# Kernel tuning notes

Measured on AMD Instinct MI355X. Metric: run time of the kernel, lower is better.

## Reference

```python
import jax, jax.numpy as jnp
import numpy as np
import math

L, B, T, S, E, H, F = 6, 8, 1024, 1024, 1024, 16, 4096
HD = E // H
EPS = 1e-5

def setup_inputs() -> dict:
    key = jax.random.key(0)
    ks = jax.random.split(key, 20)
    def n(k, shape, s=0.02):
        return jax.random.normal(k, shape, dtype=jnp.float32) * s
    return {
        'encoder_output': n(ks[0], (B, S, E), 1.0),
        'decoder_input': n(ks[1], (B, T, E), 1.0),
        # LayerNorm params (stacked over layers)
        'ln1_w': jnp.ones((L, E), jnp.float32), 'ln1_b': jnp.zeros((L, E), jnp.float32),
        'ln2_w': jnp.ones((L, E), jnp.float32), 'ln2_b': jnp.zeros((L, E), jnp.float32),
        'ln3_w': jnp.ones((L, E), jnp.float32), 'ln3_b': jnp.zeros((L, E), jnp.float32),
        # self-attention: per-head wq/wk/wv concatenated into [E,E] (x @ W convention)
        'Wq_s': n(ks[2], (L, E, E)), 'Wk_s': n(ks[3], (L, E, E)), 'Wv_s': n(ks[4], (L, E, E)),
        'Wo_s': n(ks[5], (L, E, E)), 'bo_s': jnp.zeros((L, E), jnp.float32),
        # cross-attention
        'Wq_c': n(ks[6], (L, E, E)), 'Wk_c': n(ks[7], (L, E, E)), 'Wv_c': n(ks[8], (L, E, E)),
        'Wo_c': n(ks[9], (L, E, E)), 'bo_c': jnp.zeros((L, E), jnp.float32),
        # FFN
        'W1': n(ks[10], (L, E, F)), 'b1': jnp.zeros((L, F), jnp.float32),
        'W2': n(ks[11], (L, F, E)), 'b2': jnp.zeros((L, E), jnp.float32),
    }

def _layernorm(x, w, b):
    m = jnp.mean(x, axis=-1, keepdims=True)
    v = jnp.mean(jnp.square(x - m), axis=-1, keepdims=True)
    return (x - m) * jax.lax.rsqrt(v + EPS) * w + b

def _split_heads(x):
    b, s, _ = x.shape
    return x.reshape(b, s, H, HD).transpose(0, 2, 1, 3)  # [B,H,S,HD]

def _mha(q_in, k_in, v_in, Wq, Wk, Wv, Wo, bo, mask):
    q = _split_heads(q_in @ Wq)
    k = _split_heads(k_in @ Wk)
    v = _split_heads(v_in @ Wv)
    scores = jnp.einsum('bhqd,bhkd->bhqk', q, k) / math.sqrt(HD)
    if mask is not None:
        scores = jnp.where(mask, scores, jnp.float32(-jnp.inf))
    attn = jax.nn.softmax(scores, axis=-1)
    out = jnp.einsum('bhqk,bhkd->bhqd', attn, v)
    out = out.transpose(0, 2, 1, 3).reshape(q_in.shape[0], q_in.shape[1], E)
    return out @ Wo + bo

def reference(encoder_output, decoder_input,
              ln1_w, ln1_b, ln2_w, ln2_b, ln3_w, ln3_b,
              Wq_s, Wk_s, Wv_s, Wo_s, bo_s,
              Wq_c, Wk_c, Wv_c, Wo_c, bo_c,
              W1, b1, W2, b2):
    causal = jnp.tril(jnp.ones((T, T), dtype=bool))  # [T,T] -> broadcast over B,H
    params = (ln1_w, ln1_b, ln2_w, ln2_b, ln3_w, ln3_b,
              Wq_s, Wk_s, Wv_s, Wo_s, bo_s,
              Wq_c, Wk_c, Wv_c, Wo_c, bo_c,
              W1, b1, W2, b2)

    def layer(x, p):
        (l1w, l1b, l2w, l2b, l3w, l3b,
         wqs, wks, wvs, wos, bos,
         wqc, wkc, wvc, woc, boc,
         w1, bb1, w2, bb2) = p
        nx = _layernorm(x, l1w, l1b)
        x = x + _mha(nx, nx, nx, wqs, wks, wvs, wos, bos, causal)
        x = x + _mha(_layernorm(x, l2w, l2b), encoder_output, encoder_output,
                     wqc, wkc, wvc, woc, boc, None)
        h = _layernorm(x, l3w, l3b)
        x = x + (jax.nn.gelu(h @ w1 + bb1) @ w2 + bb2)
        return x, None

    out, _ = jax.lax.scan(layer, decoder_input, params)
    return out
```

## Files before the change

kernel.cpp:

```cpp
#include <hip/hip_runtime.h>
#include <cstdint>

typedef __bf16 bf16;
typedef __bf16 bf16x8 __attribute__((ext_vector_type(8)));
typedef __bf16 bf16x4 __attribute__((ext_vector_type(4)));
typedef float f32x4 __attribute__((ext_vector_type(4)));

static_assert(sizeof(bf16) == 2, "bf16 size");

constexpr int LAYERS = 6;
constexpr int BATCH  = 8;
constexpr int TDEC   = 1024;
constexpr int SENC   = 1024;
constexpr int EMB    = 1024;
constexpr int NH     = 16;
constexpr int FFN    = 4096;
constexpr int MTOK   = BATCH * TDEC;

typedef __attribute__((address_space(1))) void gvoid;
typedef __attribute__((address_space(3))) void lvoid;

__device__ __forceinline__ void gload16(const void* g, void* l) {
  __builtin_amdgcn_global_load_lds((gvoid*)(uintptr_t)g,
                                   (lvoid*)(uint32_t)(uintptr_t)l,
                                   16, 0, 0);
}

__device__ __forceinline__ f32x4 mfma_16x16x32(bf16x8 a, bf16x8 b, f32x4 c) {
  return __builtin_amdgcn_mfma_f32_16x16x32_bf16(a, b, c, 0, 0, 0);
}

__global__ void k_cvt(const float* __restrict__ in, bf16* __restrict__ outp, int n4) {
  int i = blockIdx.x * 256 + threadIdx.x;
  if (i < n4) {
    float4 v = ((const float4*)in)[i];
    bf16x4 o;
    o[0] = (bf16)v.x; o[1] = (bf16)v.y; o[2] = (bf16)v.z; o[3] = (bf16)v.w;
    ((bf16x4*)outp)[i] = o;
  }
}

__launch_bounds__(256)
__global__ void k_transpose(const float* __restrict__ in, bf16* __restrict__ outp,
                            int R, int C) {
  __shared__ float tile[32][33];
  const int tx = threadIdx.x, ty = threadIdx.y;
  const int r0 = blockIdx.y * 32, c0 = blockIdx.x * 32;
#pragma unroll
  for (int i = 0; i < 32; i += 8)
    tile[ty + i][tx] = in[(size_t)(r0 + ty + i) * C + c0 + tx];
  __syncthreads();
#pragma unroll
  for (int i = 0; i < 32; i += 8)
    outp[(size_t)(c0 + ty + i) * R + r0 + tx] = (bf16)tile[tx][ty + i];
}

__launch_bounds__(256)
__global__ void k_transpose4(const float* __restrict__ s0, const float* __restrict__ s1,
                             const float* __restrict__ s2, const float* __restrict__ s3,
                             bf16* __restrict__ d0, bf16* __restrict__ d1,
                             bf16* __restrict__ d2, bf16* __restrict__ d3,
                             int R, int C) {
  const int z = blockIdx.z;
  const float* in = (z == 0) ? s0 : (z == 1) ? s1 : (z == 2) ? s2 : s3;
  bf16* outp      = (z == 0) ? d0 : (z == 1) ? d1 : (z == 2) ? d2 : d3;
  __shared__ float tile[32][33];
  const int tx = threadIdx.x, ty = threadIdx.y;
  const int r0 = blockIdx.y * 32, c0 = blockIdx.x * 32;
#pragma unroll
  for (int i = 0; i < 32; i += 8)
    tile[ty + i][tx] = in[(size_t)(r0 + ty + i) * C + c0 + tx];
  __syncthreads();
#pragma unroll
  for (int i = 0; i < 32; i += 8)
    outp[(size_t)(c0 + ty + i) * R + r0 + tx] = (bf16)tile[tx][ty + i];
}

__launch_bounds__(256)
__global__ void k_layernorm(const float* __restrict__ x, const float* __restrict__ w,
                            const float* __restrict__ bb, bf16* __restrict__ outp) {
  const int row = blockIdx.x;
  const int t = threadIdx.x;
  const float4 v = ((const float4*)(x + (size_t)row * EMB))[t];
  float s = v.x + v.y + v.z + v.w;
  __shared__ float red[4];
#pragma unroll
  for (int off = 32; off > 0; off >>= 1) s += __shfl_down(s, off, 64);
  if ((t & 63) == 0) red[t >> 6] = s;
  __syncthreads();
  const float mean = (red[0] + red[1] + red[2] + red[3]) * (1.0f / EMB);
  const float dx = v.x - mean, dy = v.y - mean, dz = v.z - mean, dw = v.w - mean;
  float ss = dx * dx + dy * dy + dz * dz + dw * dw;
  __syncthreads();
#pragma unroll
  for (int off = 32; off > 0; off >>= 1) ss += __shfl_down(ss, off, 64);
  if ((t & 63) == 0) red[t >> 6] = ss;
  __syncthreads();
  const float var = (red[0] + red[1] + red[2] + red[3]) * (1.0f / EMB);
  const float rstd = rsqrtf(var + 1e-5f);
  const float4 wv = ((const float4*)w)[t];
  const float4 bv = ((const float4*)bb)[t];
  bf16x4 o;
  o[0] = (bf16)(dx * rstd * wv.x + bv.x);
  o[1] = (bf16)(dy * rstd * wv.y + bv.y);
  o[2] = (bf16)(dz * rstd * wv.z + bv.z);
  o[3] = (bf16)(dw * rstd * wv.w + bv.w);
  *(bf16x4*)(outp + (size_t)row * EMB + t * 4) = o;
}

template <int EPI>
__launch_bounds__(256)
__global__ void k_gemm(const bf16* __restrict__ A, const bf16* __restrict__ Bt,
                       int M, int N, int K, int ldc,
                       bf16* __restrict__ outb, float* __restrict__ outf,
                       const float* __restrict__ res, const float* __restrict__ bias) {
  __shared__ __align__(16) bf16 sA[128 * 32];
  __shared__ __align__(16) bf16 sB[128 * 32];
  const int tid = threadIdx.x;
  const int wave = tid >> 6, lane = tid & 63;
  const int quad = lane >> 4, l16 = lane & 15;
  const int wm = wave >> 1, wn = wave & 1;

  int bid = blockIdx.y * gridDim.x + blockIdx.x;
  const int nwg = gridDim.x * gridDim.y;
  if ((nwg & 7) == 0) {
    const int q = nwg >> 3;
    bid = (bid & 7) * q + (bid >> 3);
  }
  const int bn = bid % gridDim.x;
  const int bm = bid / gridDim.x;

  f32x4 acc[4][4] = {};

  const int srow = wave * 16 + (lane >> 2);
  const int scol = (lane & 3) * 8;
  const bf16* Ag = A  + (size_t)(bm * 128 + srow) * K + scol;
  const bf16* Bg = Bt + (size_t)(bn * 128 + srow) * K + scol;
  bf16* sA0 = &sA[(wave * 16) * 32];
  bf16* sA1 = &sA[(wave * 16 + 64) * 32];
  bf16* sB0 = &sB[(wave * 16) * 32];
  bf16* sB1 = &sB[(wave * 16 + 64) * 32];

  const int nk = K >> 5;
  for (int kt = 0; kt < nk; ++kt) {
    gload16(Ag, sA0);
    gload16(Ag + (size_t)64 * K, sA1);
    gload16(Bg, sB0);
    gload16(Bg + (size_t)64 * K, sB1);
    Ag += 32; Bg += 32;
    __syncthreads();
    bf16x8 af[4], bfv[4];
    const bf16* pa = &sA[(wm * 64 + l16) * 32 + quad * 8];
    const bf16* pb = &sB[(wn * 64 + l16) * 32 + quad * 8];
#pragma unroll
    for (int i = 0; i < 4; ++i) af[i] = *(const bf16x8*)(pa + i * 16 * 32);
#pragma unroll
    for (int i = 0; i < 4; ++i) bfv[i] = *(const bf16x8*)(pb + i * 16 * 32);
#pragma unroll
    for (int i = 0; i < 4; ++i)
#pragma unroll
      for (int j = 0; j < 4; ++j)
        acc[i][j] = mfma_16x16x32(af[i], bfv[j], acc[i][j]);
    __syncthreads();
  }

  const int row0 = bm * 128 + wm * 64;
  const int col0 = bn * 128 + wn * 64;
#pragma unroll
  for (int j = 0; j < 4; ++j) {
    const int c = col0 + j * 16 + l16;
    const float bv = (EPI >= 1) ? bias[c] : 0.0f;
#pragma unroll
    for (int i = 0; i < 4; ++i) {
#pragma unroll
      for (int r = 0; r < 4; ++r) {
        const size_t rr = (size_t)(row0 + i * 16 + quad * 4 + r);
        float v = acc[i][j][r];
        if (EPI == 0) {
          outb[rr * ldc + c] = (bf16)v;
        } else if (EPI == 1) {
          v += bv;
          const float u = 0.7978845608028654f * (v + 0.044715f * v * v * v);
          const float g = v / (1.0f + exp2f(u * -2.8853900817779268f));
          outb[rr * ldc + c] = (bf16)g;
        } else {
          outf[rr * ldc + c] = res[rr * ldc + c] + v + bv;
        }
      }
    }
  }
}

template <bool CAUSAL>
__launch_bounds__(256)
__global__ void k_attn(const bf16* __restrict__ Q, const bf16* __restrict__ Kg,
                       const bf16* __restrict__ Vg, bf16* __restrict__ Og,
                       int TQ, int TK, int ld) {
  __shared__ __align__(16) bf16 sK[64 * 64];
  __shared__ __align__(16) bf16 sVt[64 * 72];
  __shared__ __align__(16) bf16 sP[4][32 * 72];
  const int tid = threadIdx.x;
  const int wave = tid >> 6, lane = tid & 63;
  const int quad = lane >> 4, l16 = lane & 15;

  int bx = blockIdx.x, by = blockIdx.y;
  {
    const int nwg = gridDim.x * gridDim.y;
    if ((nwg & 7) == 0 && (gridDim.y & 7) == 0) {
      const int d = by * gridDim.x + bx;
      const int xcd = d & 7, idx = d >> 3;
      const int hpx = gridDim.y >> 3;
      by = xcd * hpx + idx / gridDim.x;
      bx = idx % gridDim.x;
    }
  }
  const int b = by >> 4;
  const int h = by & 15;
  const int qt = CAUSAL ? (gridDim.x - 1 - bx) : bx;
  const int q0 = qt * 128;
  const int qw = q0 + wave * 32;

  const bf16* Qbase = Q + (size_t)(b * TQ) * ld + h * 64;
  const bf16* Kbase = Kg + (size_t)(b * TK) * ld + h * 64;
  const bf16* Vbase = Vg + (size_t)(b * TK) * ld + h * 64;

  bf16x8 aq[2][2];
#pragma unroll
  for (int m = 0; m < 2; ++m) {
    const bf16* qp = Qbase + (size_t)(qw + m * 16 + l16) * ld + quad * 8;
    aq[m][0] = *(const bf16x8*)(qp);
    aq[m][1] = *(const bf16x8*)(qp + 32);
  }

  f32x4 oacc[2][4] = {};
  float m_[2][4], l_[2][4];
#pragma unroll
  for (int m = 0; m < 2; ++m)
#pragma unroll
    for (int r = 0; r < 4; ++r) { m_[m][r] = -1e30f; l_[m][r] = 0.0f; }

  const int srow = lane >> 3;
  const int schunk = lane & 7;
  bf16* sPw = &sP[wave][0];

  const float sc = 0.125f * 1.44269504088896f;
  const int nj = CAUSAL ? (q0 >> 6) + 2 : (TK >> 6);

  for (int j = 0; j < nj; ++j) {
    const int k0 = j * 64;
#pragma unroll
    for (int r2 = 0; r2 < 2; ++r2) {
      const int rowt = (wave + 4 * r2) * 8 + srow;
      const int gchunk = schunk ^ (rowt & 7);
      gload16(Kbase + (size_t)(k0 + rowt) * ld + gchunk * 8,
              &sK[(wave + 4 * r2) * 8 * 64]);
    }
#pragma unroll
    for (int r2 = 0; r2 < 2; ++r2) {
      const int cv = wave + 4 * r2;
      const bf16x8 vv = *(const bf16x8*)(Vbase + (size_t)(k0 + lane) * ld + cv * 8);
#pragma unroll
      for (int e = 0; e < 8; ++e) sVt[(cv * 8 + e) * 72 + lane] = vv[e];
    }
    __syncthreads();

    const bool active = !CAUSAL || (k0 <= qw + 31);
    if (active) {
#pragma unroll
      for (int m = 0; m < 2; ++m) {
        f32x4 s[4];
#pragma unroll
        for (int kt = 0; kt < 4; ++kt) {
          const int krow = kt * 16 + l16;
          const int p0 = (quad ^ (l16 & 7)) * 8;
          const int p1 = ((quad + 4) ^ (l16 & 7)) * 8;
          const bf16x8 bk0 = *(const bf16x8*)(&sK[krow * 64 + p0]);
          const bf16x8 bk1 = *(const bf16x8*)(&sK[krow * 64 + p1]);
          f32x4 z = {};
          z = mfma_16x16x32(aq[m][0], bk0, z);
          z = mfma_16x16x32(aq[m][1], bk1, z);
          s[kt] = z;
        }
        float rowmax[4] = {-1e30f, -1e30f, -1e30f, -1e30f};
#pragma unroll
        for (int kt = 0; kt < 4; ++kt) {
          const int key = k0 + kt * 16 + l16;
#pragma unroll
          for (int r = 0; r < 4; ++r) {
            if (CAUSAL && key > qw + m * 16 + quad * 4 + r) s[kt][r] = -1e30f;
            rowmax[r] = fmaxf(rowmax[r], s[kt][r]);
          }
        }
#pragma unroll
        for (int off = 1; off < 16; off <<= 1)
#pragma unroll
          for (int r = 0; r < 4; ++r)
            rowmax[r] = fmaxf(rowmax[r], __shfl_xor(rowmax[r], off, 64));
        float alpha[4], nms[4], rs[4];
#pragma unroll
        for (int r = 0; r < 4; ++r) {
          const float mn = fmaxf(m_[m][r], rowmax[r]);
          alpha[r] = exp2f((m_[m][r] - mn) * sc);
          m_[m][r] = mn;
          nms[r] = -mn * sc;
          rs[r] = 0.0f;
        }
#pragma unroll
        for (int kt = 0; kt < 4; ++kt)
#pragma unroll
          for (int r = 0; r < 4; ++r) {
            const float pv = exp2f(fmaf(s[kt][r], sc, nms[r]));
            rs[r] += pv;
            sPw[(m * 16 + quad * 4 + r) * 72 + kt * 16 + l16] = (bf16)pv;
          }
#pragma unroll
        for (int off = 1; off < 16; off <<= 1)
#pragma unroll
          for (int r = 0; r < 4; ++r)
            rs[r] += __shfl_xor(rs[r], off, 64);
#pragma unroll
        for (int r = 0; r < 4; ++r) {
          l_[m][r] = l_[m][r] * alpha[r] + rs[r];
#pragma unroll
          for (int dt = 0; dt < 4; ++dt) oacc[m][dt][r] *= alpha[r];
        }
        const bf16x8 ap0 = *(const bf16x8*)(&sPw[(m * 16 + l16) * 72 + quad * 8]);
        const bf16x8 ap1 = *(const bf16x8*)(&sPw[(m * 16 + l16) * 72 + 32 + quad * 8]);
#pragma unroll
        for (int dt = 0; dt < 4; ++dt) {
          const bf16x8 bv0 = *(const bf16x8*)(&sVt[(dt * 16 + l16) * 72 + quad * 8]);
          const bf16x8 bv1 = *(const bf16x8*)(&sVt[(dt * 16 + l16) * 72 + 32 + quad * 8]);
          oacc[m][dt] = mfma_16x16x32(ap0, bv0, oacc[m][dt]);
          oacc[m][dt] = mfma_16x16x32(ap1, bv1, oacc[m][dt]);
        }
      }
    }
    __syncthreads();
  }

#pragma unroll
  for (int m = 0; m < 2; ++m)
#pragma unroll
    for (int r = 0; r < 4; ++r) {
      const float inv = 1.0f / l_[m][r];
      bf16* op = Og + (size_t)(b * TQ + qw + m * 16 + quad * 4 + r) * EMB + h * 64;
#pragma unroll
      for (int dt = 0; dt < 4; ++dt)
        op[dt * 16 + l16] = (bf16)(oacc[m][dt][r] * inv);
    }
}

extern "C" void kernel_launch(void* const* d_in, const int* in_sizes, int n_in,
                              void* d_out, int out_size, void* d_ws, size_t ws_size,
                              hipStream_t stream) {
  const float* enc  = (const float*)d_in[0];
  const float* dec  = (const float*)d_in[1];
  const float* ln1w = (const float*)d_in[2];
  const float* ln1b = (const float*)d_in[3];
  const float* ln2w = (const float*)d_in[4];
  const float* ln2b = (const float*)d_in[5];
  const float* ln3w = (const float*)d_in[6];
  const float* ln3b = (const float*)d_in[7];
  const float* Wq_s = (const float*)d_in[8];
  const float* Wk_s = (const float*)d_in[9];
  const float* Wv_s = (const float*)d_in[10];
  const float* Wo_s = (const float*)d_in[11];
  const float* bo_s = (const float*)d_in[12];
  const float* Wq_c = (const float*)d_in[13];
  const float* Wk_c = (const float*)d_in[14];
  const float* Wv_c = (const float*)d_in[15];
  const float* Wo_c = (const float*)d_in[16];
  const float* bo_c = (const float*)d_in[17];
  const float* W1   = (const float*)d_in[18];
  const float* b1   = (const float*)d_in[19];
  const float* W2   = (const float*)d_in[20];
  const float* b2   = (const float*)d_in[21];
  float* out = (float*)d_out;

  char* p = (char*)d_ws;
  auto take = [&](size_t bytes) {
    char* r = p;
    p += (bytes + 255) & ~(size_t)255;
    return (void*)r;
  };
  bf16* wqkvT = (bf16*)take((size_t)3 * EMB * EMB * 2);
  bf16* woT   = (bf16*)take((size_t)EMB * EMB * 2);
  bf16* w1T   = (bf16*)take((size_t)EMB * FFN * 2);
  bf16* w2T   = (bf16*)take((size_t)FFN * EMB * 2);
  bf16* encb  = (bf16*)take((size_t)BATCH * SENC * EMB * 2);
  float* xbuf = (float*)take((size_t)MTOK * EMB * 4);
  bf16* nx    = (bf16*)take((size_t)MTOK * EMB * 2);
  bf16* qkvb  = (bf16*)take((size_t)MTOK * 3 * EMB * 2);
  bf16* ab    = (bf16*)take((size_t)MTOK * EMB * 2);
  bf16* hb    = (bf16*)take((size_t)MTOK * FFN * 2);
  if ((size_t)((char*)p - (char*)d_ws) > ws_size) return;

  const int LD3 = 3 * EMB;

  {
    const int n4 = BATCH * SENC * EMB / 4;
    k_cvt<<<(n4 + 255) / 256, 256, 0, stream>>>(enc, encb, n4);
  }
  hipMemcpyAsync(xbuf, dec, (size_t)MTOK * EMB * 4, hipMemcpyDeviceToDevice, stream);

  auto trans = [&](const float* w, bf16* wt, int R, int C) {
    k_transpose<<<dim3(C / 32, R / 32), dim3(32, 8), 0, stream>>>(w, wt, R, C);
  };
  auto trans4 = [&](const float* s0, const float* s1, const float* s2, const float* s3,
                    bf16* d0, bf16* d1, bf16* d2, bf16* d3) {
    k_transpose4<<<dim3(EMB / 32, EMB / 32, 4), dim3(32, 8), 0, stream>>>(
        s0, s1, s2, s3, d0, d1, d2, d3, EMB, EMB);
  };
  auto gemm0 = [&](const bf16* Ap, const bf16* Btp, bf16* op, int M, int N, int K,
                   int ldc) {
    k_gemm<0><<<dim3(N / 128, M / 128), 256, 0, stream>>>(Ap, Btp, M, N, K, ldc, op,
                                                          nullptr, nullptr, nullptr);
  };
  auto gemm_gelu = [&](const bf16* Ap, const bf16* Btp, bf16* op, const float* bi,
                       int M, int N, int K) {
    k_gemm<1><<<dim3(N / 128, M / 128), 256, 0, stream>>>(Ap, Btp, M, N, K, N, op,
                                                          nullptr, nullptr, bi);
  };
  auto gemm_res = [&](const bf16* Ap, const bf16* Btp, float* op, const float* rs,
                      const float* bi, int M, int N, int K) {
    k_gemm<2><<<dim3(N / 128, M / 128), 256, 0, stream>>>(Ap, Btp, M, N, K, N, nullptr,
                                                          op, rs, bi);
  };

  for (int l = 0; l < LAYERS; ++l) {
    const size_t wofs = (size_t)l * EMB * EMB;
    k_layernorm<<<MTOK, 256, 0, stream>>>(xbuf, ln1w + l * EMB, ln1b + l * EMB, nx);
    trans4(Wq_s + wofs, Wk_s + wofs, Wv_s + wofs, Wo_s + wofs,
           wqkvT, wqkvT + (size_t)EMB * EMB, wqkvT + (size_t)2 * EMB * EMB, woT);
    gemm0(nx, wqkvT, qkvb, MTOK, 3 * EMB, EMB, LD3);
    k_attn<true><<<dim3(TDEC / 128, BATCH * NH), 256, 0, stream>>>(
        qkvb, qkvb + EMB, qkvb + 2 * EMB, ab, TDEC, TDEC, LD3);
    gemm_res(ab, woT, xbuf, xbuf, bo_s + l * EMB, MTOK, EMB, EMB);

    k_layernorm<<<MTOK, 256, 0, stream>>>(xbuf, ln2w + l * EMB, ln2b + l * EMB, nx);
    trans4(Wq_c + wofs, Wk_c + wofs, Wv_c + wofs, Wo_c + wofs,
           wqkvT, wqkvT + (size_t)EMB * EMB, wqkvT + (size_t)2 * EMB * EMB, woT);
    gemm0(nx, wqkvT, qkvb, MTOK, EMB, EMB, LD3);
    gemm0(encb, wqkvT + (size_t)EMB * EMB, qkvb + EMB, BATCH * SENC, 2 * EMB, EMB, LD3);
    k_attn<false><<<dim3(TDEC / 128, BATCH * NH), 256, 0, stream>>>(
        qkvb, qkvb + EMB, qkvb + 2 * EMB, ab, TDEC, SENC, LD3);
    gemm_res(ab, woT, xbuf, xbuf, bo_c + l * EMB, MTOK, EMB, EMB);

    k_layernorm<<<MTOK, 256, 0, stream>>>(xbuf, ln3w + l * EMB, ln3b + l * EMB, nx);
    trans(W1 + (size_t)l * EMB * FFN, w1T, EMB, FFN);
    trans(W2 + (size_t)l * FFN * EMB, w2T, FFN, EMB);
    gemm_gelu(nx, w1T, hb, b1 + (size_t)l * FFN, MTOK, FFN, EMB);
    float* fout = (l == LAYERS - 1) ? out : xbuf;
    gemm_res(hb, w2T, fout, xbuf, b2 + (size_t)l * EMB, MTOK, EMB, FFN);
  }
}
```

Measured before the change: 4.881 ms.

## Double-buffer attention K/V tiles and compute softmax row sums via MFMA

The attention kernel now double-buffers the K and V shared-memory tiles. It prefetches the next tile (async LDS load for K, registers for V) while the current tile is computed, which removes one barrier per iteration and hides global load latency. The row-sum shuffle reduction is replaced by an MFMA against a vector of ones, and the causal mask is applied only on diagonal tiles. In exchange, shared memory use and register pressure go up, which may reduce occupancy. The row sum now comes from the bf16-rounded probabilities.

New measurement: 4.594 ms. 5.9% less time.

```diff
diff --git a/kernel.cpp b/kernel.cpp
--- a/kernel.cpp
+++ b/kernel.cpp
@@ -196,8 +196,8 @@
 __global__ void k_attn(const bf16* __restrict__ Q, const bf16* __restrict__ Kg,
                        const bf16* __restrict__ Vg, bf16* __restrict__ Og,
                        int TQ, int TK, int ld) {
-  __shared__ __align__(16) bf16 sK[64 * 64];
-  __shared__ __align__(16) bf16 sVt[64 * 72];
+  __shared__ __align__(16) bf16 sK[2][64 * 64];
+  __shared__ __align__(16) bf16 sVt[2][64 * 72];
   __shared__ __align__(16) bf16 sP[4][32 * 72];
   const int tid = threadIdx.x;
   const int wave = tid >> 6, lane = tid & 63;
@@ -232,6 +232,10 @@
     aq[m][1] = *(const bf16x8*)(qp + 32);
   }
 
+  bf16x8 vones;
+#pragma unroll
+  for (int e = 0; e < 8; ++e) vones[e] = (bf16)1.0f;
+
   f32x4 oacc[2][4] = {};
   float m_[2][4], l_[2][4];
 #pragma unroll
@@ -246,23 +250,42 @@
   const float sc = 0.125f * 1.44269504088896f;
   const int nj = CAUSAL ? (q0 >> 6) + 2 : (TK >> 6);
 
+#pragma unroll
+  for (int r2 = 0; r2 < 2; ++r2) {
+    const int rowt = (wave + 4 * r2) * 8 + srow;
+    const int gchunk = schunk ^ (rowt & 7);
+    gload16(Kbase + (size_t)rowt * ld + gchunk * 8,
+            &sK[0][(wave + 4 * r2) * 8 * 64]);
+  }
+#pragma unroll
+  for (int r2 = 0; r2 < 2; ++r2) {
+    const int cv = wave + 4 * r2;
+    const bf16x8 vv = *(const bf16x8*)(Vbase + (size_t)lane * ld + cv * 8);
+#pragma unroll
+    for (int e = 0; e < 8; ++e) sVt[0][(cv * 8 + e) * 72 + lane] = vv[e];
+  }
+  __syncthreads();
+
+  int cur = 0;
   for (int j = 0; j < nj; ++j) {
+    const int nxt = cur ^ 1;
     const int k0 = j * 64;
-#pragma unroll
-    for (int r2 = 0; r2 < 2; ++r2) {
-      const int rowt = (wave + 4 * r2) * 8 + srow;
-      const int gchunk = schunk ^ (rowt & 7);
-      gload16(Kbase + (size_t)(k0 + rowt) * ld + gchunk * 8,
-              &sK[(wave + 4 * r2) * 8 * 64]);
-    }
-#pragma unroll
-    for (int r2 = 0; r2 < 2; ++r2) {
-      const int cv = wave + 4 * r2;
-      const bf16x8 vv = *(const bf16x8*)(Vbase + (size_t)(k0 + lane) * ld + cv * 8);
-#pragma unroll
-      for (int e = 0; e < 8; ++e) sVt[(cv * 8 + e) * 72 + lane] = vv[e];
-    }
-    __syncthreads();
+    const bool pre = (j + 1 < nj);
+    bf16x8 vpre[2];
+    if (pre) {
+      const int k0n = k0 + 64;
+#pragma unroll
+      for (int r2 = 0; r2 < 2; ++r2) {
+        const int rowt = (wave + 4 * r2) * 8 + srow;
+        const int gchunk = schunk ^ (rowt & 7);
+        gload16(Kbase + (size_t)(k0n + rowt) * ld + gchunk * 8,
+                &sK[nxt][(wave + 4 * r2) * 8 * 64]);
+      }
+#pragma unroll
+      for (int r2 = 0; r2 < 2; ++r2)
+        vpre[r2] = *(const bf16x8*)(Vbase + (size_t)(k0n + lane) * ld +
+                                    (wave + 4 * r2) * 8);
+    }
 
     const bool active = !CAUSAL || (k0 <= qw + 31);
     if (active) {
@@ -274,68 +297,83 @@
           const int krow = kt * 16 + l16;
           const int p0 = (quad ^ (l16 & 7)) * 8;
           const int p1 = ((quad + 4) ^ (l16 & 7)) * 8;
-          const bf16x8 bk0 = *(const bf16x8*)(&sK[krow * 64 + p0]);
-          const bf16x8 bk1 = *(const bf16x8*)(&sK[krow * 64 + p1]);
+          const bf16x8 bk0 = *(const bf16x8*)(&sK[cur][krow * 64 + p0]);
+          const bf16x8 bk1 = *(const bf16x8*)(&sK[cur][krow * 64 + p1]);
           f32x4 z = {};
           z = mfma_16x16x32(aq[m][0], bk0, z);
           z = mfma_16x16x32(aq[m][1], bk1, z);
           s[kt] = z;
         }
+        const int row_base = qw + m * 16;
         float rowmax[4] = {-1e30f, -1e30f, -1e30f, -1e30f};
-#pragma unroll
-        for (int kt = 0; kt < 4; ++kt) {
-          const int key = k0 + kt * 16 + l16;
-#pragma unroll
-          for (int r = 0; r < 4; ++r) {
-            if (CAUSAL && key > qw + m * 16 + quad * 4 + r) s[kt][r] = -1e30f;
-            rowmax[r] = fmaxf(rowmax[r], s[kt][r]);
+        if (CAUSAL && (k0 + 63 > row_base)) {
+#pragma unroll
+          for (int kt = 0; kt < 4; ++kt) {
+            const int key = k0 + kt * 16 + l16;
+#pragma unroll
+            for (int r = 0; r < 4; ++r) {
+              if (key > row_base + quad * 4 + r) s[kt][r] = -1e30f;
+              rowmax[r] = fmaxf(rowmax[r], s[kt][r]);
+            }
           }
+        } else {
+#pragma unroll
+          for (int kt = 0; kt < 4; ++kt)
+#pragma unroll
+            for (int r = 0; r < 4; ++r)
+              rowmax[r] = fmaxf(rowmax[r], s[kt][r]);
         }
 #pragma unroll
         for (int off = 1; off < 16; off <<= 1)
 #pragma unroll
           for (int r = 0; r < 4; ++r)
             rowmax[r] = fmaxf(rowmax[r], __shfl_xor(rowmax[r], off, 64));
-        float alpha[4], nms[4], rs[4];
+        float alpha[4], nms[4];
 #pragma unroll
         for (int r = 0; r < 4; ++r) {
           const float mn = fmaxf(m_[m][r], rowmax[r]);
           alpha[r] = exp2f((m_[m][r] - mn) * sc);
           m_[m][r] = mn;
           nms[r] = -mn * sc;
-          rs[r] = 0.0f;
         }
 #pragma unroll
         for (int kt = 0; kt < 4; ++kt)
 #pragma unroll
           for (int r = 0; r < 4; ++r) {
             const float pv = exp2f(fmaf(s[kt][r], sc, nms[r]));
-            rs[r] += pv;
             sPw[(m * 16 + quad * 4 + r) * 72 + kt * 16 + l16] = (bf16)pv;
           }
-#pragma unroll
-        for (int off = 1; off < 16; off <<= 1)
-#pragma unroll
-          for (int r = 0; r < 4; ++r)
-            rs[r] += __shfl_xor(rs[r], off, 64);
-#pragma unroll
-        for (int r = 0; r < 4; ++r) {
-          l_[m][r] = l_[m][r] * alpha[r] + rs[r];
-#pragma unroll
-          for (int dt = 0; dt < 4; ++dt) oacc[m][dt][r] *= alpha[r];
-        }
         const bf16x8 ap0 = *(const bf16x8*)(&sPw[(m * 16 + l16) * 72 + quad * 8]);
         const bf16x8 ap1 = *(const bf16x8*)(&sPw[(m * 16 + l16) * 72 + 32 + quad * 8]);
+        f32x4 zs = {};
+        zs = mfma_16x16x32(ap0, vones, zs);
+        zs = mfma_16x16x32(ap1, vones, zs);
+#pragma unroll
+        for (int r = 0; r < 4; ++r) {
+          l_[m][r] = l_[m][r] * alpha[r] + zs[r];
+#pragma unroll
+          for (int dt = 0; dt < 4; ++dt) oacc[m][dt][r] *= alpha[r];
+        }
 #pragma unroll
         for (int dt = 0; dt < 4; ++dt) {
-          const bf16x8 bv0 = *(const bf16x8*)(&sVt[(dt * 16 + l16) * 72 + quad * 8]);
-          const bf16x8 bv1 = *(const bf16x8*)(&sVt[(dt * 16 + l16) * 72 + 32 + quad * 8]);
+          const bf16x8 bv0 = *(const bf16x8*)(&sVt[cur][(dt * 16 + l16) * 72 + quad * 8]);
+          const bf16x8 bv1 = *(const bf16x8*)(&sVt[cur][(dt * 16 + l16) * 72 + 32 + quad * 8]);
           oacc[m][dt] = mfma_16x16x32(ap0, bv0, oacc[m][dt]);
           oacc[m][dt] = mfma_16x16x32(ap1, bv1, oacc[m][dt]);
         }
       }
     }
+
+    if (pre) {
+#pragma unroll
+      for (int r2 = 0; r2 < 2; ++r2) {
+        const int cv = wave + 4 * r2;
+#pragma unroll
+        for (int e = 0; e < 8; ++e) sVt[nxt][(cv * 8 + e) * 72 + lane] = vpre[r2][e];
+      }
+    }
     __syncthreads();
+    cur = nxt;
   }
 
 #pragma unroll
```
